# Kernel optimization log

Measured on AMD Instinct MI355X. Metric: run time of the kernel, lower is better.

Reference implementation:

```python
import jax, jax.numpy as jnp
import numpy as np

B, P, K, E, H, V, C = 128, 64, 64, 300, 300, 50000, 3


def lstm0(x, Wih, bih, bhh):
    # PyTorch LSTMCell single step with zero initial (h, c) state.
    # gates = x @ Wih^T + bih + Whh @ 0 + bhh ; chunks order: i, f, g, o
    g = x @ Wih.T + bih + bhh
    i, f, gg, o = jnp.split(g, 4, axis=-1)
    c = jax.nn.sigmoid(i) * jnp.tanh(gg)
    return jax.nn.sigmoid(o) * jnp.tanh(c)


def setup_inputs() -> dict:
    key = jax.random.key(0)
    ks = jax.random.split(key, 24)
    d = {}
    d["premise"] = jax.random.randint(ks[0], (B, P), 1, V)
    d["premise_len"] = jax.random.randint(ks[1], (B,), P // 2, P + 1)
    d["hypothesis"] = jax.random.randint(ks[2], (B, K), 1, V)
    d["hypothesis_len"] = jax.random.randint(ks[3], (B,), K // 2, K + 1)
    embed = jax.random.normal(ks[4], (V, E), jnp.float32) * 0.1
    d["embed"] = embed.at[0].set(0.0)  # padding_idx=0
    d["w_e"] = jax.random.uniform(ks[5], (H,), jnp.float32)
    xav = (2.0 / (H + H)) ** 0.5
    d["W_s"] = jax.random.normal(ks[6], (H, H), jnp.float32) * xav
    d["W_t"] = jax.random.normal(ks[7], (H, H), jnp.float32) * xav
    d["W_m"] = jax.random.normal(ks[8], (H, H), jnp.float32) * xav
    d["fc_w"] = jax.random.normal(ks[9], (C, H), jnp.float32) * (2.0 / (H + C)) ** 0.5
    d["fc_b"] = jax.random.uniform(ks[10], (C,), jnp.float32)
    s = 1.0 / np.sqrt(H)
    def cell(k1, k2, k3, k4, in_dim):
        return (jax.random.uniform(k1, (4 * H, in_dim), jnp.float32, -s, s),
                jax.random.uniform(k2, (4 * H, H), jnp.float32, -s, s),
                jax.random.uniform(k3, (4 * H,), jnp.float32, -s, s),
                jax.random.uniform(k4, (4 * H,), jnp.float32, -s, s))
    d["Wih_p"], d["Whh_p"], d["bih_p"], d["bhh_p"] = cell(ks[11], ks[12], ks[13], ks[14], E)
    d["Wih_h"], d["Whh_h"], d["bih_h"], d["bhh_h"] = cell(ks[15], ks[16], ks[17], ks[18], E)
    d["Wih_m"], d["Whh_m"], d["bih_m"], d["bhh_m"] = cell(ks[19], ks[20], ks[21], ks[22], 2 * H)
    return d


def reference(premise, premise_len, hypothesis, hypothesis_len, embed, w_e,
              W_s, W_t, W_m, fc_w, fc_b,
              Wih_p, Whh_p, bih_p, bhh_p,
              Wih_h, Whh_h, bih_h, bhh_h,
              Wih_m, Whh_m, bih_m, bhh_m):
    prem_emb = embed[premise]      # [B,P,E]
    hypo_emb = embed[hypothesis]   # [B,K,E]
    # Original code calls LSTMCell on a whole sequence -> per-token single step
    # with zero initial state (no temporal recurrence in these two cells).
    h_s = lstm0(prem_emb, Wih_p, bih_p, bhh_p)  # [B,P,H]
    h_t = lstm0(hypo_emb, Wih_h, bih_h, bhh_h)  # [B,K,H]
    s_proj = h_s @ W_s.T                         # [B,P,H]
    t_proj = jnp.transpose(h_t @ W_t.T, (1, 0, 2))  # [K,B,H]
    h_t_kb = jnp.transpose(h_t, (1, 0, 2))          # [K,B,H]
    b, p = h_s.shape[0], h_s.shape[1]
    pmask = jnp.arange(p)[None, :] < premise_len[:, None]  # [B,P]
    neg = jnp.finfo(s_proj.dtype).min

    def step(h_m, xs):
        t_k, ht_k = xs  # [B,H], [B,H]
        m_proj = h_m @ W_m.T  # [B,H]
        e = jnp.einsum('bph,h->bp',
                       jnp.tanh(s_proj + t_k[:, None, :] + m_proj[:, None, :]), w_e)
        e = jnp.where(pmask, e, neg)
        alpha = jax.nn.softmax(e, axis=1)           # softmax over valid premise pos
        a = jnp.einsum('bp,bph->bh', alpha, h_s)    # attention-weighted premise
        m = jnp.concatenate([a, ht_k], axis=-1)     # [B,2H]
        # lstm_match is re-invoked with zero state each k in the original
        h_m_new = lstm0(m, Wih_m, bih_m, bhh_m)
        return h_m_new, h_m_new

    _, hs_all = jax.lax.scan(step, jnp.zeros((b, s_proj.shape[-1]), s_proj.dtype),
                             (t_proj, h_t_kb))      # [K,B,H]
    h_fin = hs_all[hypothesis_len - 1, jnp.arange(b)]  # h_m at last valid hypo step
    logits = h_fin @ fc_w.T + fc_b
    return jax.nn.softmax(logits, axis=1)
```

## Files before the change

kernel.cpp:

```cpp
#include <hip/hip_runtime.h>
#include <stdint.h>

typedef unsigned short u16;
typedef __attribute__((ext_vector_type(8))) __bf16 bf16x8;
typedef __attribute__((ext_vector_type(4))) float f32x4;

__device__ __forceinline__ float bf2f(u16 u) {
    union { unsigned int i; float f; } v; v.i = ((unsigned int)u) << 16; return v.f;
}
__device__ __forceinline__ float bf2f_lo(unsigned int u) {
    union { unsigned int i; float f; } v; v.i = u << 16; return v.f;
}
__device__ __forceinline__ float bf2f_hi(unsigned int u) {
    union { unsigned int i; float f; } v; v.i = u & 0xffff0000u; return v.f;
}
__device__ __forceinline__ u16 f2bf(float f) {
    union { float f; unsigned int i; } v; v.f = f;
    unsigned int x = v.i;
    unsigned int r = (x + 0x7fffu + ((x >> 16) & 1u)) >> 16;
    return (u16)r;
}
__device__ __forceinline__ float rdf(const void* p, size_t i, int isbf) {
    return isbf ? bf2f(((const u16*)p)[i]) : ((const float*)p)[i];
}
__device__ __forceinline__ float fast_sigmoid(float x) {
    return __builtin_amdgcn_rcpf(1.f + __expf(-x));
}
__device__ __forceinline__ float fast_tanh(float x) {
    float u = __expf(x + x);
    return 1.f - 2.f * __builtin_amdgcn_rcpf(u + 1.f);
}
__device__ __forceinline__ bf16x8 as_bf8(uint4 u) {
    union { uint4 a; bf16x8 b; } c; c.a = u; return c.b;
}
__device__ __forceinline__ float rdlane_f(float v, int l) {
    return __int_as_float(__builtin_amdgcn_readlane(__float_as_int(v), l));
}

#define BB 128
#define PP 64
#define KK 64
#define HH 300
#define MROWS 8192
#define KPAD 320
#define N3H 900
#define GLD 912
#define NT1 19
#define NT4 57
#define NW 16

__global__ void detect_dtype(const u16* __restrict__ raw, int* __restrict__ flag) {
    __shared__ int cnt;
    if (threadIdx.x == 0) cnt = 0;
    __syncthreads();
    if (threadIdx.x < 300 && (raw[threadIdx.x] & 0x8000u)) atomicAdd(&cnt, 1);
    __syncthreads();
    if (threadIdx.x == 0) *flag = (cnt < 8) ? 1 : 0;
}

__global__ void pack_w(const void* __restrict__ src, u16* __restrict__ dst,
                       int dstRowsPad, int nsrcRows, int srcld, int colOff, int igo,
                       const int* __restrict__ flag) {
    int i = blockIdx.x * 256 + threadIdx.x;
    if (i >= dstRowsPad * KPAD) return;
    int isbf = *flag;
    int r = i / KPAD, c = i % KPAD;
    u16 v = 0;
    if (r < nsrcRows && c < HH) {
        int sr = igo ? (r < HH ? r : r + HH) : r;
        v = f2bf(rdf(src, (size_t)sr * srcld + colOff + c, isbf));
    }
    dst[i] = v;
}

__global__ void pack_w_gates(const void* __restrict__ Wp, const void* __restrict__ Wh,
                             const void* __restrict__ Wm,
                             u16* __restrict__ dp, u16* __restrict__ dh,
                             u16* __restrict__ da, u16* __restrict__ dm2,
                             const int* __restrict__ flag) {
    int i = blockIdx.x * 256 + threadIdx.x;
    if (i >= 1024 * KPAD) return;
    int y = blockIdx.y;
    int isbf = *flag;
    const void* src = (y == 0) ? Wp : (y == 1) ? Wh : Wm;
    u16* dst = (y == 0) ? dp : (y == 1) ? dh : (y == 2) ? da : dm2;
    int srcld = (y < 2) ? HH : 600;
    int colOff = (y == 3) ? HH : 0;
    int r = i / KPAD, c = i % KPAD;
    u16 v = 0;
    if (r < N3H && c < HH) {
        int sr = (r < HH) ? r : r + HH;
        v = f2bf(rdf(src, (size_t)sr * srcld + colOff + c, isbf));
    }
    dst[i] = v;
}

__global__ void pack_wf(const void* __restrict__ Wm, uint4* __restrict__ dst,
                        const int* __restrict__ flag) {
    int i = blockIdx.x * 256 + threadIdx.x;
    if (i >= NT1 * 10 * 64) return;
    int isbf = *flag;
    int lane = i & 63, ks = (i >> 6) % 10, T = i / 640;
    int j = T * 16 + (lane & 15);
    int k0 = 32 * ks + 8 * (lane >> 4);
    unsigned int d[4];
    #pragma unroll
    for (int q = 0; q < 4; ++q) {
        int ka = k0 + 2 * q, kb = k0 + 2 * q + 1;
        unsigned int lo = (j < 300 && ka < 300) ? f2bf(rdf(Wm, (size_t)j * HH + ka, isbf)) : 0;
        unsigned int hi = (j < 300 && kb < 300) ? f2bf(rdf(Wm, (size_t)j * HH + kb, isbf)) : 0;
        d[q] = lo | (hi << 16);
    }
    uint4 v; v.x = d[0]; v.y = d[1]; v.z = d[2]; v.w = d[3];
    dst[i] = v;
}

__global__ void pack_bias(const void* bip, const void* bhp, const void* bih_, const void* bhh_,
                          const void* bim, const void* bhm,
                          float* bp, float* bh, float* bm, const int* __restrict__ flag) {
    int i = blockIdx.x * 256 + threadIdx.x;
    if (i >= 3 * N3H) return;
    int isbf = *flag;
    int which = i / N3H, r = i % N3H;
    int sr = (r < HH) ? r : r + HH;
    if (which == 0)      bp[r] = rdf(bip, sr, isbf) + rdf(bhp, sr, isbf);
    else if (which == 1) bh[r] = rdf(bih_, sr, isbf) + rdf(bhh_, sr, isbf);
    else                 bm[r] = rdf(bim, sr, isbf) + rdf(bhm, sr, isbf);
}

__global__ void pack_we(const void* __restrict__ we, float* __restrict__ dst,
                        const int* __restrict__ flag) {
    int i = threadIdx.x;
    dst[i] = (i < 300) ? 2.f * rdf(we, i, *flag) : 0.f;
}

__global__ void gather_embed(const int* __restrict__ idx, const void* __restrict__ embed,
                             u16* __restrict__ X, const int* __restrict__ flag) {
    int i = blockIdx.x * 256 + threadIdx.x;
    int isbf = *flag;
    int r = i / KPAD, c = i % KPAD;
    X[i] = (c < HH) ? f2bf(rdf(embed, (size_t)idx[r] * HH + c, isbf)) : (u16)0;
}

__global__ void zero_out(u16* out) { out[threadIdx.x] = 0; }

__global__ __launch_bounds__(256) void gemm_bt(
    const u16* __restrict__ A, const u16* __restrict__ B,
    u16* __restrict__ Cb, const float* __restrict__ bias, int N, int ldc, int frag)
{
    __shared__ __align__(16) u16 At[128 * 32];
    __shared__ __align__(16) u16 Bt[128 * 32];
    const int tid = threadIdx.x;
    const int m0 = blockIdx.x * 128;
    const int n0 = blockIdx.y * 128;
    const int lane = tid & 63;
    const int wave = tid >> 6;
    const int rm = (wave & 1) * 64;
    const int rn = (wave >> 1) * 64;
    const int qr = lane >> 4;
    const int lr = lane & 15;

    f32x4 acc[4][4] = {};

    const int c0 = tid, c1 = tid + 256;
    const int r0 = c0 >> 2, o0 = (c0 & 3) * 8;
    const int r1 = c1 >> 2, o1 = (c1 & 3) * 8;

    for (int k0 = 0; k0 < KPAD; k0 += 32) {
        uint4 a0v = *(const uint4*)(A + (size_t)(m0 + r0) * KPAD + k0 + o0);
        uint4 a1v = *(const uint4*)(A + (size_t)(m0 + r1) * KPAD + k0 + o1);
        uint4 b0v = *(const uint4*)(B + (size_t)(n0 + r0) * KPAD + k0 + o0);
        uint4 b1v = *(const uint4*)(B + (size_t)(n0 + r1) * KPAD + k0 + o1);
        __syncthreads();
        *(uint4*)(At + c0 * 8) = a0v;
        *(uint4*)(At + c1 * 8) = a1v;
        *(uint4*)(Bt + c0 * 8) = b0v;
        *(uint4*)(Bt + c1 * 8) = b1v;
        __syncthreads();
        bf16x8 af[4], bfr[4];
        #pragma unroll
        for (int i = 0; i < 4; ++i) {
            af[i]  = *(const bf16x8*)(At + (rm + i * 16 + lr) * 32 + qr * 8);
            bfr[i] = *(const bf16x8*)(Bt + (rn + i * 16 + lr) * 32 + qr * 8);
        }
        #pragma unroll
        for (int mi = 0; mi < 4; ++mi)
            #pragma unroll
            for (int ni = 0; ni < 4; ++ni)
                acc[mi][ni] = __builtin_amdgcn_mfma_f32_16x16x32_bf16(
                    af[mi], bfr[ni], acc[mi][ni], 0, 0, 0);
    }
    #pragma unroll
    for (int mi = 0; mi < 4; ++mi) {
        #pragma unroll
        for (int ni = 0; ni < 4; ++ni) {
            int n = n0 + rn + ni * 16 + lr;
            int mb = m0 + rm + mi * 16 + qr * 4;
            if (!frag) {
                if (n >= ldc) continue;
                if (n < N) {
                    float bv = bias ? bias[n] : 0.f;
                    #pragma unroll
                    for (int r = 0; r < 4; ++r)
                        Cb[(size_t)(mb + r) * ldc + n] = f2bf(acc[mi][ni][r] + bv);
                } else {
                    #pragma unroll
                    for (int r = 0; r < 4; ++r)
                        Cb[(size_t)(mb + r) * ldc + n] = 0;
                }
            } else {
                if (n >= GLD) continue;
                int bb = mb >> 6, p0 = mb & 63;
                size_t base = ((((size_t)bb * NT4 + (n >> 4)) * 2 + (p0 >> 5)) * 64
                               + ((p0 >> 3) & 3) * 16 + (n & 15)) * 8 + (p0 & 7);
                u16 wv[4];
                if (n < N) {
                    float bv = bias ? bias[n] : 0.f;
                    #pragma unroll
                    for (int r = 0; r < 4; ++r) wv[r] = f2bf(acc[mi][ni][r] + bv);
                } else {
                    #pragma unroll
                    for (int r = 0; r < 4; ++r) wv[r] = 0;
                }
                uint2 st;
                st.x = (unsigned int)wv[0] | ((unsigned int)wv[1] << 16);
                st.y = (unsigned int)wv[2] | ((unsigned int)wv[3] << 16);
                *(uint2*)(Cb + base) = st;
            }
        }
    }
}

__global__ void lstm_act(const u16* __restrict__ gates, u16* __restrict__ hout) {
    int idx = blockIdx.x * 256 + threadIdx.x;
    int r = idx / KPAD, c = idx % KPAD;
    float h = 0.f;
    if (c < HH) {
        const u16* g = gates + (size_t)r * N3H;
        float gi = bf2f(g[c]);
        float gg = bf2f(g[c + HH]);
        float go = bf2f(g[c + 2 * HH]);
        float cc = fast_sigmoid(gi) * fast_tanh(gg);
        h = fast_sigmoid(go) * fast_tanh(cc);
    }
    hout[idx] = f2bf(h);
}

__global__ __launch_bounds__(1024, 1) void scan_kernel(
    const u16* __restrict__ sproj,
    const u16* __restrict__ tproj,
    const uint4* __restrict__ Gmf,
    const u16* __restrict__ hp,
    const uint4* __restrict__ Wf,
    const float* __restrict__ we2g,
    const int* __restrict__ premise_len,
    const int* __restrict__ hypothesis_len,
    float* __restrict__ hfin)
{
    __shared__ __align__(16) uint4 gml[NT4 * 2 * 64];
    __shared__ __align__(16) uint4 wlds[3 * 10 * 64];
    __shared__ __align__(16) unsigned int hmhi[160];
    __shared__ __align__(16) unsigned int hmlo[160];
    __shared__ __align__(16) float part[NW][64];
    __shared__ __align__(16) u16 aw_sh[128];
    __shared__ __align__(16) float gates[912];

    const int b = blockIdx.x, t = threadIdx.x;
    const int lane = t & 63, w = t >> 6;
    const int lr = lane & 15, qr = lane >> 4;
    const int plen = premise_len[b], hlen = hypothesis_len[b];

    {
        const uint4* gsrc = Gmf + (size_t)b * (NT4 * 2 * 64);
        for (int i = t; i < NT4 * 2 * 64; i += 1024) gml[i] = gsrc[i];
    }
    for (int i = t; i < 3 * 10 * 64; i += 1024) wlds[i] = Wf[16 * 640 + i];
    if (t < 160) { hmhi[t] = 0; hmlo[t] = 0; }

    uint4 wreg[10];
    #pragma unroll
    for (int ks = 0; ks < 10; ++ks) wreg[ks] = Wf[(size_t)w * 640 + ks * 64 + lane];

    const int wu = __builtin_amdgcn_readfirstlane(w);
    const bool hasB = (wu < 3);
    unsigned int spdA[8], spdB[8];
    {
        const u16* srow = sproj + (size_t)(b * PP + lane) * KPAD;
        uint4 v0 = *(const uint4*)(srow + 16 * wu);
        uint4 v1 = *(const uint4*)(srow + 16 * wu + 8);
        spdA[0] = v0.x; spdA[1] = v0.y; spdA[2] = v0.z; spdA[3] = v0.w;
        spdA[4] = v1.x; spdA[5] = v1.y; spdA[6] = v1.z; spdA[7] = v1.w;
        uint4 v2 = *(const uint4*)(srow + 256 + 16 * wu);
        uint4 v3 = *(const uint4*)(srow + 256 + 16 * wu + 8);
        spdB[0] = v2.x; spdB[1] = v2.y; spdB[2] = v2.z; spdB[3] = v2.w;
        spdB[4] = v3.x; spdB[5] = v3.y; spdB[6] = v3.z; spdB[7] = v3.w;
    }
    float weA[16], weB[16];
    {
        const float* wA = we2g + 16 * wu;
        const float* wB = we2g + 256 + 16 * wu;
        #pragma unroll
        for (int j = 0; j < 16; ++j) { weA[j] = wA[j]; weB[j] = wB[j]; }
    }

    float wsumf = 0.f;
    if (w == 0) {
        float s = 0.f;
        #pragma unroll
        for (int q = 0; q < 5; ++q) s += we2g[lane + 64 * q];
        #pragma unroll
        for (int d = 32; d; d >>= 1) s += __shfl_xor(s, d);
        wsumf = 0.5f * s;
    }
    __syncthreads();

    const int nt4 = (w < 9) ? 4 : 3;
    const bool act2 = lane < plen;

    for (int k = 0; k < hlen; ++k) {
        const u16* tprow = tproj + (size_t)(b * KK + k) * KPAD;
        const u16* hprow = hp + (size_t)(b * KK + k) * 900;

        u16 hpv[4];
        #pragma unroll
        for (int i = 0; i < 4; ++i) {
            hpv[i] = 0;
            if (i < nt4 && lane < 16) {
                int j = (w + 16 * i) * 16 + lane;
                if (j < 900) hpv[i] = hprow[j];
            }
        }
        u16 tk0 = 0, tk1 = 0;
        if (lane < 16) {
            tk0 = tprow[w * 16 + lane];
            if (hasB) tk1 = tprow[(16 + w) * 16 + lane];
        }

        float vcolA, vcolB;
        {
            const unsigned int* abase = (lr == 1) ? hmlo : hmhi;
            uint4 z; z.x = 0; z.y = 0; z.z = 0; z.w = 0;
            f32x4 r0 = {}, r1 = {}, l0 = {}, l1 = {};
            #pragma unroll
            for (int h = 0; h < 2; ++h) {
                bf16x8 a1[5];
                #pragma unroll
                for (int j = 0; j < 5; ++j) {
                    int ks = 5 * h + j;
                    uint4 u = *(const uint4*)(abase + 16 * ks + 4 * qr);
                    a1[j] = as_bf8((lr < 2) ? u : z);
                }
                #pragma unroll
                for (int j = 0; j < 5; ++j) {
                    int ks = 5 * h + j;
                    if (j & 1) r1 = __builtin_amdgcn_mfma_f32_16x16x32_bf16(a1[j], as_bf8(wreg[ks]), r1, 0, 0, 0);
                    else       r0 = __builtin_amdgcn_mfma_f32_16x16x32_bf16(a1[j], as_bf8(wreg[ks]), r0, 0, 0, 0);
                }
                if (hasB) {
                    #pragma unroll
                    for (int j = 0; j < 5; ++j) {
                        int ks = 5 * h + j;
                        bf16x8 bb = as_bf8(wlds[wu * 640 + ks * 64 + lane]);
                        if (j & 1) l1 = __builtin_amdgcn_mfma_f32_16x16x32_bf16(a1[j], bb, l1, 0, 0, 0);
                        else       l0 = __builtin_amdgcn_mfma_f32_16x16x32_bf16(a1[j], bb, l0, 0, 0, 0);
                    }
                }
            }
            vcolA = 2.f * (bf2f(tk0) + ((r0[0] + r0[1]) + (r1[0] + r1[1])));
            vcolB = 2.f * (bf2f(tk1) + ((l0[0] + l0[1]) + (l1[0] + l1[1])));
        }

        {
            float accn = 0.f;
            if (act2) {
                #pragma unroll
                for (int c = 0; c < 16; ++c) {
                    float xc = rdlane_f(vcolA, c);
                    float spv = (c & 1) ? bf2f_hi(spdA[c >> 1]) : bf2f_lo(spdA[c >> 1]);
                    float arg = fmaf(2.f, spv, xc);
                    accn = fmaf(weA[c], __builtin_amdgcn_rcpf(__expf(arg) + 1.f), accn);
                }
                if (hasB) {
                    #pragma unroll
                    for (int c = 0; c < 16; ++c) {
                        float xc = rdlane_f(vcolB, c);
                        float spv = (c & 1) ? bf2f_hi(spdB[c >> 1]) : bf2f_lo(spdB[c >> 1]);
                        float arg = fmaf(2.f, spv, xc);
                        accn = fmaf(weB[c], __builtin_amdgcn_rcpf(__expf(arg) + 1.f), accn);
                    }
                }
            }
            part[w][lane] = act2 ? accn : 0.f;
        }
        __syncthreads();

        if (w == 0) {
            float s = 0.f;
            #pragma unroll
            for (int q = 0; q < NW; ++q) s += part[q][lane];
            float e = act2 ? (wsumf - s) : -1e30f;
            float mx = e;
            #pragma unroll
            for (int d = 32; d; d >>= 1) mx = fmaxf(mx, __shfl_xor(mx, d));
            float ex = act2 ? __expf(e - mx) : 0.f;
            float sm = ex;
            #pragma unroll
            for (int d = 32; d; d >>= 1) sm += __shfl_xor(sm, d);
            float al = ex * __builtin_amdgcn_rcpf(sm);
            u16 ah = f2bf(al);
            aw_sh[lane] = ah;
            aw_sh[64 + lane] = f2bf(al - bf2f(ah));
        }
        __syncthreads();

        bf16x8 a4[2];
        {
            const u16* abase = aw_sh + ((lr == 1) ? 64 : 0);
            uint4 z; z.x = 0; z.y = 0; z.z = 0; z.w = 0;
            #pragma unroll
            for (int ks = 0; ks < 2; ++ks) {
                uint4 u = *(const uint4*)(abase + 32 * ks + 8 * qr);
                a4[ks] = as_bf8((lr < 2) ? u : z);
            }
        }
        #pragma unroll
        for (int i = 0; i < 4; ++i) {
            if (i < nt4) {
                int T = w + 16 * i;
                f32x4 ac0 = {}, ac1 = {};
                ac0 = __builtin_amdgcn_mfma_f32_16x16x32_bf16(a4[0], as_bf8(gml[(T * 2 + 0) * 64 + lane]), ac0, 0, 0, 0);
                ac1 = __builtin_amdgcn_mfma_f32_16x16x32_bf16(a4[1], as_bf8(gml[(T * 2 + 1) * 64 + lane]), ac1, 0, 0, 0);
                if (lane < 16) gates[T * 16 + lane] = ((ac0[0] + ac0[1]) + (ac1[0] + ac1[1])) + bf2f(hpv[i]);
            }
        }
        __syncthreads();

        if (t < 300) {
            float gi = gates[t], gg = gates[300 + t], go = gates[600 + t];
            float cc = fast_sigmoid(gi) * fast_tanh(gg);
            float h = fast_sigmoid(go) * fast_tanh(cc);
            if (k == hlen - 1) hfin[(size_t)b * KPAD + t] = h;
            u16 hh = f2bf(h);
            float res = h - bf2f(hh);
            float hn = __shfl_down(h, 1);
            float rn2 = __shfl_down(res, 1);
            if ((t & 1) == 0) {
                hmhi[t >> 1] = (unsigned int)hh | ((unsigned int)f2bf(hn) << 16);
                hmlo[t >> 1] = (unsigned int)f2bf(res) | ((unsigned int)f2bf(rn2) << 16);
            }
        }
        __syncthreads();
    }
}

__global__ void fc_softmax(const float* __restrict__ hfin, const void* __restrict__ fcw,
                           const void* __restrict__ fcb, void* __restrict__ out,
                           const int* __restrict__ flag) {
    __shared__ float lg[128][3];
    int t = threadIdx.x;
    int b = t & 127, c = t >> 7;
    int isbf = *flag;
    {
        float acc = rdf(fcb, c, isbf);
        const float* hr = hfin + (size_t)b * KPAD;
        for (int h = 0; h < HH; ++h) acc += hr[h] * rdf(fcw, (size_t)c * HH + h, isbf);
        lg[b][c] = acc;
    }
    __syncthreads();
    if (t < 128) {
        float l0 = lg[t][0], l1 = lg[t][1], l2 = lg[t][2];
        float mx = fmaxf(l0, fmaxf(l1, l2));
        float e0 = __expf(l0 - mx), e1 = __expf(l1 - mx), e2 = __expf(l2 - mx);
        float inv = __builtin_amdgcn_rcpf(e0 + e1 + e2);
        if (isbf) {
            u16* o = (u16*)out;
            o[t * 3 + 0] = f2bf(e0 * inv);
            o[t * 3 + 1] = f2bf(e1 * inv);
            o[t * 3 + 2] = f2bf(e2 * inv);
        } else {
            float* o = (float*)out;
            o[t * 3 + 0] = e0 * inv;
            o[t * 3 + 1] = e1 * inv;
            o[t * 3 + 2] = e2 * inv;
        }
    }
}

extern "C" void kernel_launch(void* const* d_in, const int* in_sizes, int n_in,
                              void* d_out, int out_size, void* d_ws, size_t ws_size,
                              hipStream_t stream) {
    const int* premise        = (const int*)d_in[0];
    const int* premise_len    = (const int*)d_in[1];
    const int* hypothesis     = (const int*)d_in[2];
    const int* hypothesis_len = (const int*)d_in[3];
    const void* embed = d_in[4];
    const void* w_e   = d_in[5];
    const void* W_s   = d_in[6];
    const void* W_t   = d_in[7];
    const void* W_m   = d_in[8];
    const void* fc_w  = d_in[9];
    const void* fc_b  = d_in[10];
    const void* Wih_p = d_in[11];
    const void* bih_p = d_in[13];
    const void* bhh_p = d_in[14];
    const void* Wih_h = d_in[15];
    const void* bih_h = d_in[17];
    const void* bhh_h = d_in[18];
    const void* Wih_m = d_in[19];
    const void* bih_m = d_in[21];
    const void* bhh_m = d_in[22];
    (void)in_sizes; (void)n_in; (void)out_size;

    char* w = (char*)d_ws;
    auto alloc = [&](size_t bytes) -> char* {
        char* r = (char*)(((uintptr_t)w + 255) & ~(uintptr_t)255);
        w = r + bytes;
        return r;
    };
    char* regA = alloc((size_t)MROWS * KPAD * 2);
    char* regB = alloc((size_t)MROWS * GLD * 2);
    char* regC = alloc((size_t)MROWS * N3H * 2);
    char* regD = alloc((size_t)MROWS * KPAD * 2);
    char* regE = alloc((size_t)MROWS * KPAD * 2);
    u16* Wp_pad  = (u16*)alloc((size_t)1024 * KPAD * 2);
    u16* Wh_pad  = (u16*)alloc((size_t)1024 * KPAD * 2);
    u16* Wa_pad  = (u16*)alloc((size_t)1024 * KPAD * 2);
    u16* Whm_pad = (u16*)alloc((size_t)1024 * KPAD * 2);
    u16* Ws_pad  = (u16*)alloc((size_t)384 * KPAD * 2);
    u16* Wt_pad  = (u16*)alloc((size_t)384 * KPAD * 2);
    uint4* Wf    = (uint4*)alloc((size_t)NT1 * 10 * 64 * 16);
    float* we2g  = (float*)alloc(320 * 4);
    float* bsum_p = (float*)alloc(N3H * 4);
    float* bsum_h = (float*)alloc(N3H * 4);
    float* bsum_m = (float*)alloc(N3H * 4);
    int* dflag   = (int*)alloc(256);
    size_t needed = (size_t)(w - (char*)d_ws);
    if (needed > ws_size) {
        zero_out<<<1, 384, 0, stream>>>((u16*)d_out);
        return;
    }
    u16* Xbuf   = (u16*)regA;
    u16* s_proj = (u16*)regA;
    u16* h_s    = (u16*)regD;
    u16* t_proj = (u16*)regD;
    u16* h_t    = (u16*)regE;
    float* h_fin = (float*)regE;

    detect_dtype<<<1, 320, 0, stream>>>((const u16*)w_e, dflag);
    pack_w_gates<<<dim3(1280, 4), 256, 0, stream>>>(Wih_p, Wih_h, Wih_m,
                                                    Wp_pad, Wh_pad, Wa_pad, Whm_pad, dflag);
    pack_w<<<480, 256, 0, stream>>>(W_s, Ws_pad, 384, HH, HH, 0, 0, dflag);
    pack_w<<<480, 256, 0, stream>>>(W_t, Wt_pad, 384, HH, HH, 0, 0, dflag);
    pack_wf<<<48, 256, 0, stream>>>(W_m, Wf, dflag);
    pack_we<<<1, 320, 0, stream>>>(w_e, we2g, dflag);
    pack_bias<<<11, 256, 0, stream>>>(bih_p, bhh_p, bih_h, bhh_h, bih_m, bhh_m,
                                      bsum_p, bsum_h, bsum_m, dflag);

    gather_embed<<<10240, 256, 0, stream>>>(premise, embed, Xbuf, dflag);
    gemm_bt<<<dim3(64, 8), 256, 0, stream>>>(Xbuf, Wp_pad, (u16*)regB, bsum_p, N3H, N3H, 0);
    lstm_act<<<10240, 256, 0, stream>>>((u16*)regB, h_s);
    gather_embed<<<10240, 256, 0, stream>>>(hypothesis, embed, Xbuf, dflag);
    gemm_bt<<<dim3(64, 8), 256, 0, stream>>>(Xbuf, Wh_pad, (u16*)regC, bsum_h, N3H, N3H, 0);
    lstm_act<<<10240, 256, 0, stream>>>((u16*)regC, h_t);

    gemm_bt<<<dim3(64, 3), 256, 0, stream>>>(h_s, Ws_pad, s_proj, nullptr, HH, KPAD, 0);
    gemm_bt<<<dim3(64, 8), 256, 0, stream>>>(h_s, Wa_pad, (u16*)regB, nullptr, N3H, 0, 1);
    gemm_bt<<<dim3(64, 3), 256, 0, stream>>>(h_t, Wt_pad, t_proj, nullptr, HH, KPAD, 0);
    gemm_bt<<<dim3(64, 8), 256, 0, stream>>>(h_t, Whm_pad, (u16*)regC, bsum_m, N3H, N3H, 0);

    scan_kernel<<<BB, 1024, 0, stream>>>(s_proj, t_proj, (const uint4*)regB,
                                         (const u16*)regC, Wf, we2g,
                                         premise_len, hypothesis_len, h_fin);
    fc_softmax<<<1, 384, 0, stream>>>(h_fin, fc_w, fc_b, d_out, dflag);
}
```

Measured before the change: 590.1 us.

## Batch premise/hypothesis encoder kernels and use direct global-to-LDS loads in GEMM

```diff
diff --git a/kernel.cpp b/kernel.cpp
--- a/kernel.cpp
+++ b/kernel.cpp
@@ -134,27 +134,41 @@
     dst[i] = (i < 300) ? 2.f * rdf(we, i, *flag) : 0.f;
 }
 
-__global__ void gather_embed(const int* __restrict__ idx, const void* __restrict__ embed,
-                             u16* __restrict__ X, const int* __restrict__ flag) {
+__global__ void gather_embed2(const int* __restrict__ idxP, const int* __restrict__ idxH,
+                              const void* __restrict__ embed,
+                              u16* __restrict__ XP, u16* __restrict__ XH,
+                              const int* __restrict__ flag) {
     int i = blockIdx.x * 256 + threadIdx.x;
     int isbf = *flag;
     int r = i / KPAD, c = i % KPAD;
-    X[i] = (c < HH) ? f2bf(rdf(embed, (size_t)idx[r] * HH + c, isbf)) : (u16)0;
+    const int* idx = idxP; u16* X = XP; int rr = r;
+    if (r >= MROWS) { idx = idxH; X = XH; rr = r - MROWS; }
+    u16 v = (c < HH) ? f2bf(rdf(embed, (size_t)idx[rr] * HH + c, isbf)) : (u16)0;
+    X[(size_t)rr * KPAD + c] = v;
 }
 
 __global__ void zero_out(u16* out) { out[threadIdx.x] = 0; }
 
 __global__ __launch_bounds__(256) void gemm_bt(
     const u16* __restrict__ A, const u16* __restrict__ B,
-    u16* __restrict__ Cb, const float* __restrict__ bias, int N, int ldc, int frag)
+    u16* __restrict__ Cb, const float* __restrict__ bias, int N, int ldc, int frag,
+    const u16* __restrict__ A2, const u16* __restrict__ B2,
+    u16* __restrict__ Cb2, const float* __restrict__ bias2)
 {
     __shared__ __align__(16) u16 At[128 * 32];
     __shared__ __align__(16) u16 Bt[128 * 32];
     const int tid = threadIdx.x;
-    const int m0 = blockIdx.x * 128;
+    int bx = blockIdx.x;
+    const u16* Ause = A; const u16* Buse = B; u16* Cuse = Cb; const float* buse = bias;
+    if (A2 != nullptr) {
+        int half = gridDim.x >> 1;
+        if (bx >= half) { bx -= half; Ause = A2; Buse = B2; Cuse = Cb2; buse = bias2; }
+    }
+    const int m0 = bx * 128;
     const int n0 = blockIdx.y * 128;
     const int lane = tid & 63;
     const int wave = tid >> 6;
+    const int wvb = wave * 64;
     const int rm = (wave & 1) * 64;
     const int rn = (wave >> 1) * 64;
     const int qr = lane >> 4;
@@ -162,20 +176,20 @@
 
     f32x4 acc[4][4] = {};
 
-    const int c0 = tid, c1 = tid + 256;
-    const int r0 = c0 >> 2, o0 = (c0 & 3) * 8;
-    const int r1 = c1 >> 2, o1 = (c1 & 3) * 8;
-
     for (int k0 = 0; k0 < KPAD; k0 += 32) {
-        uint4 a0v = *(const uint4*)(A + (size_t)(m0 + r0) * KPAD + k0 + o0);
-        uint4 a1v = *(const uint4*)(A + (size_t)(m0 + r1) * KPAD + k0 + o1);
-        uint4 b0v = *(const uint4*)(B + (size_t)(n0 + r0) * KPAD + k0 + o0);
-        uint4 b1v = *(const uint4*)(B + (size_t)(n0 + r1) * KPAD + k0 + o1);
-        __syncthreads();
-        *(uint4*)(At + c0 * 8) = a0v;
-        *(uint4*)(At + c1 * 8) = a1v;
-        *(uint4*)(Bt + c0 * 8) = b0v;
-        *(uint4*)(Bt + c1 * 8) = b1v;
+        #pragma unroll
+        for (int c = 0; c < 2; ++c) {
+            int cc = c * 256 + tid;
+            int r = cc >> 2, o = (cc & 3) * 8;
+            __builtin_amdgcn_global_load_lds(
+                (const __attribute__((address_space(1))) void*)(Ause + (size_t)(m0 + r) * KPAD + k0 + o),
+                (__attribute__((address_space(3))) void*)(At + (size_t)(c * 256 + wvb) * 8),
+                16, 0, 0);
+            __builtin_amdgcn_global_load_lds(
+                (const __attribute__((address_space(1))) void*)(Buse + (size_t)(n0 + r) * KPAD + k0 + o),
+                (__attribute__((address_space(3))) void*)(Bt + (size_t)(c * 256 + wvb) * 8),
+                16, 0, 0);
+        }
         __syncthreads();
         bf16x8 af[4], bfr[4];
         #pragma unroll
@@ -189,6 +203,7 @@
             for (int ni = 0; ni < 4; ++ni)
                 acc[mi][ni] = __builtin_amdgcn_mfma_f32_16x16x32_bf16(
                     af[mi], bfr[ni], acc[mi][ni], 0, 0, 0);
+        __syncthreads();
     }
     #pragma unroll
     for (int mi = 0; mi < 4; ++mi) {
@@ -199,14 +214,14 @@
             if (!frag) {
                 if (n >= ldc) continue;
                 if (n < N) {
-                    float bv = bias ? bias[n] : 0.f;
+                    float bv = buse ? buse[n] : 0.f;
                     #pragma unroll
                     for (int r = 0; r < 4; ++r)
-                        Cb[(size_t)(mb + r) * ldc + n] = f2bf(acc[mi][ni][r] + bv);
+                        Cuse[(size_t)(mb + r) * ldc + n] = f2bf(acc[mi][ni][r] + bv);
                 } else {
                     #pragma unroll
                     for (int r = 0; r < 4; ++r)
-                        Cb[(size_t)(mb + r) * ldc + n] = 0;
+                        Cuse[(size_t)(mb + r) * ldc + n] = 0;
                 }
             } else {
                 if (n >= GLD) continue;
@@ -215,7 +230,7 @@
                                + ((p0 >> 3) & 3) * 16 + (n & 15)) * 8 + (p0 & 7);
                 u16 wv[4];
                 if (n < N) {
-                    float bv = bias ? bias[n] : 0.f;
+                    float bv = buse ? buse[n] : 0.f;
                     #pragma unroll
                     for (int r = 0; r < 4; ++r) wv[r] = f2bf(acc[mi][ni][r] + bv);
                 } else {
@@ -225,25 +240,28 @@
                 uint2 st;
                 st.x = (unsigned int)wv[0] | ((unsigned int)wv[1] << 16);
                 st.y = (unsigned int)wv[2] | ((unsigned int)wv[3] << 16);
-                *(uint2*)(Cb + base) = st;
-            }
-        }
-    }
-}
-
-__global__ void lstm_act(const u16* __restrict__ gates, u16* __restrict__ hout) {
+                *(uint2*)(Cuse + base) = st;
+            }
+        }
+    }
+}
+
+__global__ void lstm_act2(const u16* __restrict__ g1, const u16* __restrict__ g2,
+                          u16* __restrict__ h1, u16* __restrict__ h2) {
     int idx = blockIdx.x * 256 + threadIdx.x;
     int r = idx / KPAD, c = idx % KPAD;
+    const u16* gsrc = g1; u16* ho = h1; int rr = r;
+    if (r >= MROWS) { gsrc = g2; ho = h2; rr = r - MROWS; }
     float h = 0.f;
     if (c < HH) {
-        const u16* g = gates + (size_t)r * N3H;
+        const u16* g = gsrc + (size_t)rr * N3H;
         float gi = bf2f(g[c]);
         float gg = bf2f(g[c + HH]);
         float go = bf2f(g[c + 2 * HH]);
         float cc = fast_sigmoid(gi) * fast_tanh(gg);
         h = fast_sigmoid(go) * fast_tanh(cc);
     }
-    hout[idx] = f2bf(h);
+    ho[(size_t)rr * KPAD + c] = f2bf(h);
 }
 
 __global__ __launch_bounds__(1024, 1) void scan_kernel(
@@ -539,8 +557,9 @@
         zero_out<<<1, 384, 0, stream>>>((u16*)d_out);
         return;
     }
-    u16* Xbuf   = (u16*)regA;
+    u16* XbufP  = (u16*)regA;
     u16* s_proj = (u16*)regA;
+    u16* XbufH  = (u16*)regD;
     u16* h_s    = (u16*)regD;
     u16* t_proj = (u16*)regD;
     u16* h_t    = (u16*)regE;
@@ -556,17 +575,19 @@
     pack_bias<<<11, 256, 0, stream>>>(bih_p, bhh_p, bih_h, bhh_h, bih_m, bhh_m,
                                       bsum_p, bsum_h, bsum_m, dflag);
 
-    gather_embed<<<10240, 256, 0, stream>>>(premise, embed, Xbuf, dflag);
-    gemm_bt<<<dim3(64, 8), 256, 0, stream>>>(Xbuf, Wp_pad, (u16*)regB, bsum_p, N3H, N3H, 0);
-    lstm_act<<<10240, 256, 0, stream>>>((u16*)regB, h_s);
-    gather_embed<<<10240, 256, 0, stream>>>(hypothesis, embed, Xbuf, dflag);
-    gemm_bt<<<dim3(64, 8), 256, 0, stream>>>(Xbuf, Wh_pad, (u16*)regC, bsum_h, N3H, N3H, 0);
-    lstm_act<<<10240, 256, 0, stream>>>((u16*)regC, h_t);
-
-    gemm_bt<<<dim3(64, 3), 256, 0, stream>>>(h_s, Ws_pad, s_proj, nullptr, HH, KPAD, 0);
-    gemm_bt<<<dim3(64, 8), 256, 0, stream>>>(h_s, Wa_pad, (u16*)regB, nullptr, N3H, 0, 1);
-    gemm_bt<<<dim3(64, 3), 256, 0, stream>>>(h_t, Wt_pad, t_proj, nullptr, HH, KPAD, 0);
-    gemm_bt<<<dim3(64, 8), 256, 0, stream>>>(h_t, Whm_pad, (u16*)regC, bsum_m, N3H, N3H, 0);
+    gather_embed2<<<20480, 256, 0, stream>>>(premise, hypothesis, embed, XbufP, XbufH, dflag);
+    gemm_bt<<<dim3(128, 8), 256, 0, stream>>>(XbufP, Wp_pad, (u16*)regB, bsum_p, N3H, N3H, 0,
+                                              XbufH, Wh_pad, (u16*)regC, bsum_h);
+    lstm_act2<<<20480, 256, 0, stream>>>((u16*)regB, (u16*)regC, h_s, h_t);
+
+    gemm_bt<<<dim3(64, 3), 256, 0, stream>>>(h_s, Ws_pad, s_proj, nullptr, HH, KPAD, 0,
+                                             nullptr, nullptr, nullptr, nullptr);
+    gemm_bt<<<dim3(64, 8), 256, 0, stream>>>(h_s, Wa_pad, (u16*)regB, nullptr, N3H, 0, 1,
+                                             nullptr, nullptr, nullptr, nullptr);
+    gemm_bt<<<dim3(64, 3), 256, 0, stream>>>(h_t, Wt_pad, t_proj, nullptr, HH, KPAD, 0,
+                                             nullptr, nullptr, nullptr, nullptr);
+    gemm_bt<<<dim3(64, 8), 256, 0, stream>>>(h_t, Whm_pad, (u16*)regC, bsum_m, N3H, N3H, 0,
+                                             nullptr, nullptr, nullptr, nullptr);
 
     scan_kernel<<<BB, 1024, 0, stream>>>(s_proj, t_proj, (const uint4*)regB,
                                          (const u16*)regC, Wf, we2g,
```

Measured after the change: 586.6 us. About the same (-0.6%).
